# Kernel tuning notes

Measured on AMD Instinct MI355X. Metric: run time of the kernel, lower is better.

The kernel has to match this reference:

```python
import jax, jax.numpy as jnp
import numpy as np

B, N, DIN, DOUT = 8, 2048, 256, 256
ALPHA = 0.2  # leaky relu slope
EPS = 1e-6


def setup_inputs() -> dict:
    key = jax.random.key(0)
    k1, k2, k3, k4 = jax.random.split(key, 4)
    h = jax.random.normal(k1, (B, N, DIN), dtype=jnp.float32)
    adj = jax.random.uniform(k2, (B, N, N), dtype=jnp.float32)
    # xavier_uniform with gain=1.414
    gain = 1.414
    limW = gain * np.sqrt(6.0 / (DIN + DOUT))
    W = jax.random.uniform(k3, (DIN, DOUT), minval=-limW, maxval=limW, dtype=jnp.float32)
    lima = gain * np.sqrt(6.0 / (2 * DOUT + 1))
    a = jax.random.uniform(k4, (2 * DOUT, 1), minval=-lima, maxval=lima, dtype=jnp.float32)
    return {"h": h, "adj": adj, "W": W, "a": a}


def reference(h, adj, W, a):
    # Wh: [B, N, DOUT]
    Wh = jnp.einsum("bnd,df->bnf", h, W)
    # Split additive attention: cat([Wh_i, Wh_j]) @ a == Wh_i @ a1 + Wh_j @ a2
    a1 = a[:DOUT, 0]   # [DOUT]
    a2 = a[DOUT:, 0]   # [DOUT]
    s1 = Wh @ a1       # [B, N] score contribution of source node i
    s2 = Wh @ a2       # [B, N] score contribution of target node j
    e = s1[:, :, None] + s2[:, None, :]           # [B, N, N]
    e = jnp.where(e > 0, e, ALPHA * e)            # leaky relu
    e = e + jnp.log(adj + EPS)                    # soft adjacency mask
    alpha_w = jax.nn.softmax(e, axis=-1)          # [B, N, N]
    # dropout is identity in eval / deterministic reference
    h_prime = jnp.einsum("bij,bjf->bif", alpha_w, Wh)
    return h_prime
```

## Files before the change

### kernel.cpp

```cpp
#include <hip/hip_runtime.h>
#include <hip/hip_bf16.h>
#include <stdint.h>

#define ALPHA_ 0.2f
#define EPS_   1e-6f

typedef __attribute__((ext_vector_type(8))) short  short8;
typedef __attribute__((ext_vector_type(4))) float  float4v;

static __device__ __forceinline__ unsigned short f2bf(float x) {
    union { float f; unsigned int u; } c; c.f = x;
    return (unsigned short)((c.u + 0x7fffu + ((c.u >> 16) & 1u)) >> 16);
}

#define LGKM_BARRIER() asm volatile("s_waitcnt lgkmcnt(0)\n\ts_barrier" ::: "memory")

__global__ __launch_bounds__(256) void k_wt(const float* __restrict__ W,
                                            unsigned short* __restrict__ WT) {
    const int t  = threadIdx.x;
    const int f  = blockIdx.x * 8 + (t >> 5);
    const int d0 = (t & 31) * 8;
    unsigned short v[8];
#pragma unroll
    for (int k = 0; k < 8; ++k) v[k] = f2bf(W[(d0 + k) * 256 + f]);
    uint4 o;
    o.x = (unsigned)v[0] | ((unsigned)v[1] << 16);
    o.y = (unsigned)v[2] | ((unsigned)v[3] << 16);
    o.z = (unsigned)v[4] | ((unsigned)v[5] << 16);
    o.w = (unsigned)v[6] | ((unsigned)v[7] << 16);
    *(uint4*)(WT + f * 256 + d0) = o;
}

__global__ __launch_bounds__(256) void k_wh(const float* __restrict__ h,
                                            const unsigned short* __restrict__ WT,
                                            const float* __restrict__ a,
                                            unsigned short* __restrict__ WhT,
                                            float* __restrict__ s1g,
                                            float* __restrict__ s2g) {
    __shared__ __align__(16) unsigned short A_lds[32][264];
    __shared__ float s1p[32], s2p[32];
    const int t    = threadIdx.x;
    const int lane = t & 63;
    const int wv   = t >> 6;
    const int m    = lane & 15;
    const int quad = lane >> 4;
    const int r0   = blockIdx.x * 32;
    const int b    = r0 >> 11;
    const int j0   = r0 & 2047;

    if (t < 32) { s1p[t] = 0.f; s2p[t] = 0.f; }

#pragma unroll
    for (int k = 0; k < 8; ++k) {
        const int flat = t + k * 256;
        const int r  = flat >> 6;
        const int d4 = flat & 63;
        float4v hv = *(const float4v*)(h + (size_t)(r0 + r) * 256 + d4 * 4);
        uint2 pk;
        pk.x = (unsigned)f2bf(hv.x) | ((unsigned)f2bf(hv.y) << 16);
        pk.y = (unsigned)f2bf(hv.z) | ((unsigned)f2bf(hv.w) << 16);
        *(uint2*)&A_lds[r][d4 * 4] = pk;
    }
    __syncthreads();

    const int fbase = wv * 64;
    float4v acc[2][4];
#pragma unroll
    for (int it = 0; it < 2; ++it)
#pragma unroll
        for (int ft = 0; ft < 4; ++ft)
#pragma unroll
            for (int r = 0; r < 4; ++r) acc[it][ft][r] = 0.f;

    const unsigned short* wtp = WT + (size_t)(fbase + m) * 256 + quad * 8;
    short8 bcur[4], bnxt[4];
#pragma unroll
    for (int ft = 0; ft < 4; ++ft) bcur[ft] = *(const short8*)(wtp + ft * 16 * 256);

#pragma unroll
    for (int kc = 0; kc < 8; ++kc) {
        const int kn = (kc + 1) & 7;
#pragma unroll
        for (int ft = 0; ft < 4; ++ft)
            bnxt[ft] = *(const short8*)(wtp + ft * 16 * 256 + kn * 32);
        short8 af0 = *(const short8*)&A_lds[m][kc * 32 + quad * 8];
        short8 af1 = *(const short8*)&A_lds[16 + m][kc * 32 + quad * 8];
#pragma unroll
        for (int ft = 0; ft < 4; ++ft) {
            acc[0][ft] = __builtin_amdgcn_mfma_f32_16x16x32_bf16(af0, bcur[ft], acc[0][ft], 0, 0, 0);
            acc[1][ft] = __builtin_amdgcn_mfma_f32_16x16x32_bf16(af1, bcur[ft], acc[1][ft], 0, 0, 0);
        }
#pragma unroll
        for (int ft = 0; ft < 4; ++ft) bcur[ft] = bnxt[ft];
    }

    float a1v[4], a2v[4];
#pragma unroll
    for (int ft = 0; ft < 4; ++ft) {
        a1v[ft] = a[fbase + ft * 16 + m];
        a2v[ft] = a[256 + fbase + ft * 16 + m];
    }
#pragma unroll
    for (int it = 0; it < 2; ++it) {
#pragma unroll
        for (int reg = 0; reg < 4; ++reg) {
            float v1 = 0.f, v2 = 0.f;
#pragma unroll
            for (int ft = 0; ft < 4; ++ft) {
                const float c = acc[it][ft][reg];
                v1 = fmaf(c, a1v[ft], v1);
                v2 = fmaf(c, a2v[ft], v2);
            }
            v1 += __shfl_xor(v1, 1); v2 += __shfl_xor(v2, 1);
            v1 += __shfl_xor(v1, 2); v2 += __shfl_xor(v2, 2);
            v1 += __shfl_xor(v1, 4); v2 += __shfl_xor(v2, 4);
            v1 += __shfl_xor(v1, 8); v2 += __shfl_xor(v2, 8);
            if (m == 0) {
                const int row = it * 16 + quad * 4 + reg;
                atomicAdd(&s1p[row], v1);
                atomicAdd(&s2p[row], v2);
            }
        }
    }

    unsigned short* wto = WhT + (size_t)(b * 256 + fbase) * 2048 + j0;
#pragma unroll
    for (int it = 0; it < 2; ++it)
#pragma unroll
        for (int ft = 0; ft < 4; ++ft)
#pragma unroll
            for (int reg = 0; reg < 4; ++reg)
                wto[(size_t)(ft * 16 + m) * 2048 + it * 16 + quad * 4 + reg] =
                    f2bf(acc[it][ft][reg]);

    __syncthreads();
    if (t < 32) {
        s1g[(size_t)b * 2048 + j0 + t] = s1p[t];
        s2g[(size_t)b * 2048 + j0 + t] = s2p[t];
    }
}

__global__ __launch_bounds__(256, 2) void k_attn(const float* __restrict__ adj,
                                                 const unsigned short* __restrict__ WhT,
                                                 const float* __restrict__ s1g,
                                                 const float* __restrict__ s2g,
                                                 float* __restrict__ out) {
    __shared__ __align__(16) unsigned short pbuf[2][32][136];
    __shared__ __align__(16) float s2_lds[2048];
    __shared__ float rsum_lds[32];

    const int t    = threadIdx.x;
    const int lane = t & 63;
    const int wv   = t >> 6;
    const int m    = lane & 15;
    const int quad = lane >> 4;
    const int blk  = blockIdx.x;
    const int b    = blk >> 6;
    const int i0   = (blk & 63) * 32;

    const int ip = t >> 3;
    const int jq = t & 7;

    {
        const float4v* sg = (const float4v*)(s2g + (size_t)b * 2048);
        float4v v0 = sg[t], v1 = sg[t + 256];
        ((float4v*)s2_lds)[t]       = v0;
        ((float4v*)s2_lds)[t + 256] = v1;
    }
    const float s1v = s1g[(size_t)b * 2048 + i0 + ip];
    const float* adjp = adj + (size_t)(b * 2048 + i0 + ip) * 2048 + jq * 4;

    float4v adjv[2][4];
#pragma unroll
    for (int c = 0; c < 4; ++c) adjv[0][c] = *(const float4v*)(adjp + c * 32);

    const size_t bbase = (size_t)(b * 256 + wv * 64 + m) * 2048 + quad * 8;

    float4v acc[2][4];
#pragma unroll
    for (int it = 0; it < 2; ++it)
#pragma unroll
        for (int ft = 0; ft < 4; ++ft)
#pragma unroll
            for (int r = 0; r < 4; ++r) acc[it][ft][r] = 0.f;

    float rsum = 0.f;
    __syncthreads();

#pragma unroll
    for (int step = 0; step < 16; ++step) {
        const int cur   = step & 1, nx = cur ^ 1;
        const int nstep = (step + 1) & 15;

#pragma unroll
        for (int c = 0; c < 4; ++c) {
            const float4v av  = adjv[cur][c];
            const float4v s2v = *(const float4v*)&s2_lds[step * 128 + jq * 4 + c * 32];
            float e0 = s1v + s2v.x, e1 = s1v + s2v.y, e2 = s1v + s2v.z, e3 = s1v + s2v.w;
            e0 = fmaxf(e0, ALPHA_ * e0); e1 = fmaxf(e1, ALPHA_ * e1);
            e2 = fmaxf(e2, ALPHA_ * e2); e3 = fmaxf(e3, ALPHA_ * e3);
            const float p0 = (av.x + EPS_) * __expf(e0);
            const float p1 = (av.y + EPS_) * __expf(e1);
            const float p2 = (av.z + EPS_) * __expf(e2);
            const float p3 = (av.w + EPS_) * __expf(e3);
            rsum += (p0 + p1) + (p2 + p3);
            uint2 pk;
            pk.x = (unsigned)f2bf(p0) | ((unsigned)f2bf(p1) << 16);
            pk.y = (unsigned)f2bf(p2) | ((unsigned)f2bf(p3) << 16);
            *(uint2*)&pbuf[cur][ip][jq * 4 + c * 32] = pk;
        }

#pragma unroll
        for (int c = 0; c < 4; ++c)
            adjv[nx][c] = *(const float4v*)(adjp + (size_t)nstep * 128 + c * 32);

        LGKM_BARRIER();

#pragma unroll
        for (int kc = 0; kc < 4; ++kc) {
            short8 bf[4];
#pragma unroll
            for (int ft = 0; ft < 4; ++ft)
                bf[ft] = *(const short8*)(WhT + bbase + (size_t)ft * 16 * 2048
                                          + step * 128 + kc * 32);
            short8 af0 = *(const short8*)&pbuf[cur][m][kc * 32 + quad * 8];
            short8 af1 = *(const short8*)&pbuf[cur][16 + m][kc * 32 + quad * 8];
#pragma unroll
            for (int ft = 0; ft < 4; ++ft) {
                acc[0][ft] = __builtin_amdgcn_mfma_f32_16x16x32_bf16(af0, bf[ft], acc[0][ft], 0, 0, 0);
                acc[1][ft] = __builtin_amdgcn_mfma_f32_16x16x32_bf16(af1, bf[ft], acc[1][ft], 0, 0, 0);
            }
        }
    }

    float r = rsum;
    r += __shfl_xor(r, 1); r += __shfl_xor(r, 2); r += __shfl_xor(r, 4);
    if (jq == 0) rsum_lds[ip] = r;
    __syncthreads();

#pragma unroll
    for (int it = 0; it < 2; ++it) {
#pragma unroll
        for (int reg = 0; reg < 4; ++reg) {
            const int row = it * 16 + quad * 4 + reg;
            const float inv = 1.0f / rsum_lds[row];
#pragma unroll
            for (int ft = 0; ft < 4; ++ft) {
                out[(size_t)(b * 2048 + i0 + row) * 256 + wv * 64 + ft * 16 + m] =
                    acc[it][ft][reg] * inv;
            }
        }
    }
}

extern "C" void kernel_launch(void* const* d_in, const int* in_sizes, int n_in,
                              void* d_out, int out_size, void* d_ws, size_t ws_size,
                              hipStream_t stream) {
    const float* h   = (const float*)d_in[0];
    const float* adj = (const float*)d_in[1];
    const float* W   = (const float*)d_in[2];
    const float* a   = (const float*)d_in[3];
    float* out = (float*)d_out;

    unsigned short* WhT = (unsigned short*)d_ws;
    unsigned short* WT  = (unsigned short*)((char*)d_ws + 8388608);
    float*          s1  = (float*)((char*)d_ws + 8388608 + 131072);
    float*          s2  = s1 + 16384;

    k_wt  <<<dim3(32),  dim3(256), 0, stream>>>(W, WT);
    k_wh  <<<dim3(512), dim3(256), 0, stream>>>(h, WT, a, WhT, s1, s2);
    k_attn<<<dim3(512), dim3(256), 0, stream>>>(adj, WhT, s1, s2, out);
}
```

Measured before the change: 260.6 us.

## Compute attention probabilities directly in MFMA A-fragment registers, drop LDS and barriers

The attention kernel is rebuilt so each wave computes the softmax numerators for its own 32-row tile straight in the MFMA A-operand register layout. This removes the shared-memory probability buffer and the per-step barriers. Adjacency, s2 and WhT fragments are software-pipelined through double-buffered registers, and each wave now covers 128 output features, so the grid is halved and the launch bound drops to one block per CU. Separately, the Wh kernel stages its transposed bf16 output through LDS so it can write coalesced 16-byte stores. The main risk is higher register pressure and lower occupancy: this memory-bound stream relies on fewer waves to hide latency, and the WhT loads are duplicated across the waves that share a batch.

```diff
diff --git a/kernel.cpp b/kernel.cpp
--- a/kernel.cpp
+++ b/kernel.cpp
@@ -8,12 +8,12 @@
 typedef __attribute__((ext_vector_type(8))) short  short8;
 typedef __attribute__((ext_vector_type(4))) float  float4v;
 
+union U8 { short8 s8; unsigned int u[4]; };
+
 static __device__ __forceinline__ unsigned short f2bf(float x) {
     union { float f; unsigned int u; } c; c.f = x;
     return (unsigned short)((c.u + 0x7fffu + ((c.u >> 16) & 1u)) >> 16);
 }
-
-#define LGKM_BARRIER() asm volatile("s_waitcnt lgkmcnt(0)\n\ts_barrier" ::: "memory")
 
 __global__ __launch_bounds__(256) void k_wt(const float* __restrict__ W,
                                             unsigned short* __restrict__ WT) {
@@ -38,6 +38,7 @@
                                             float* __restrict__ s1g,
                                             float* __restrict__ s2g) {
     __shared__ __align__(16) unsigned short A_lds[32][264];
+    __shared__ __align__(16) unsigned short T_lds[256][40];
     __shared__ float s1p[32], s2p[32];
     const int t    = threadIdx.x;
     const int lane = t & 63;
@@ -123,15 +124,26 @@
         }
     }
 
-    unsigned short* wto = WhT + (size_t)(b * 256 + fbase) * 2048 + j0;
 #pragma unroll
     for (int it = 0; it < 2; ++it)
 #pragma unroll
         for (int ft = 0; ft < 4; ++ft)
 #pragma unroll
             for (int reg = 0; reg < 4; ++reg)
-                wto[(size_t)(ft * 16 + m) * 2048 + it * 16 + quad * 4 + reg] =
+                T_lds[fbase + ft * 16 + m][it * 16 + quad * 4 + reg] =
                     f2bf(acc[it][ft][reg]);
+
+    {
+        uint4 o0 = *(const uint4*)&T_lds[t][0];
+        uint4 o1 = *(const uint4*)&T_lds[t][8];
+        uint4 o2 = *(const uint4*)&T_lds[t][16];
+        uint4 o3 = *(const uint4*)&T_lds[t][24];
+        unsigned short* wto = WhT + ((size_t)(b * 256 + t) * 2048) + j0;
+        *(uint4*)(wto + 0)  = o0;
+        *(uint4*)(wto + 8)  = o1;
+        *(uint4*)(wto + 16) = o2;
+        *(uint4*)(wto + 24) = o3;
+    }
 
     __syncthreads();
     if (t < 32) {
@@ -140,115 +152,114 @@
     }
 }
 
-__global__ __launch_bounds__(256, 2) void k_attn(const float* __restrict__ adj,
+static __device__ __forceinline__ uint2 pquad(float4v av, float4v s2v,
+                                              float s1, float& rs) {
+    float e0 = s1 + s2v.x, e1 = s1 + s2v.y, e2 = s1 + s2v.z, e3 = s1 + s2v.w;
+    e0 = fmaxf(e0, ALPHA_ * e0); e1 = fmaxf(e1, ALPHA_ * e1);
+    e2 = fmaxf(e2, ALPHA_ * e2); e3 = fmaxf(e3, ALPHA_ * e3);
+    const float p0 = (av.x + EPS_) * __expf(e0);
+    const float p1 = (av.y + EPS_) * __expf(e1);
+    const float p2 = (av.z + EPS_) * __expf(e2);
+    const float p3 = (av.w + EPS_) * __expf(e3);
+    rs += (p0 + p1) + (p2 + p3);
+    uint2 r;
+    r.x = (unsigned)f2bf(p0) | ((unsigned)f2bf(p1) << 16);
+    r.y = (unsigned)f2bf(p2) | ((unsigned)f2bf(p3) << 16);
+    return r;
+}
+
+__global__ __launch_bounds__(256, 1) void k_attn(const float* __restrict__ adj,
                                                  const unsigned short* __restrict__ WhT,
                                                  const float* __restrict__ s1g,
                                                  const float* __restrict__ s2g,
                                                  float* __restrict__ out) {
-    __shared__ __align__(16) unsigned short pbuf[2][32][136];
-    __shared__ __align__(16) float s2_lds[2048];
-    __shared__ float rsum_lds[32];
-
-    const int t    = threadIdx.x;
-    const int lane = t & 63;
-    const int wv   = t >> 6;
-    const int m    = lane & 15;
-    const int quad = lane >> 4;
-    const int blk  = blockIdx.x;
-    const int b    = blk >> 6;
-    const int i0   = (blk & 63) * 32;
-
-    const int ip = t >> 3;
-    const int jq = t & 7;
-
-    {
-        const float4v* sg = (const float4v*)(s2g + (size_t)b * 2048);
-        float4v v0 = sg[t], v1 = sg[t + 256];
-        ((float4v*)s2_lds)[t]       = v0;
-        ((float4v*)s2_lds)[t + 256] = v1;
-    }
-    const float s1v = s1g[(size_t)b * 2048 + i0 + ip];
-    const float* adjp = adj + (size_t)(b * 2048 + i0 + ip) * 2048 + jq * 4;
-
-    float4v adjv[2][4];
-#pragma unroll
-    for (int c = 0; c < 4; ++c) adjv[0][c] = *(const float4v*)(adjp + c * 32);
-
-    const size_t bbase = (size_t)(b * 256 + wv * 64 + m) * 2048 + quad * 8;
-
-    float4v acc[2][4];
+    const int t     = threadIdx.x;
+    const int lane  = t & 63;
+    const int wv    = t >> 6;
+    const int m     = lane & 15;
+    const int quad  = lane >> 4;
+    const int fhalf = wv & 1;
+    const int itile = blockIdx.x * 2 + (wv >> 1);
+    const int b     = itile >> 6;
+    const int i0    = (itile & 63) * 32;
+
+    const float* adjp0 = adj + (size_t)(b * 2048 + i0 + m) * 2048 + quad * 8;
+    const float* adjp1 = adjp0 + 16 * 2048;
+    const float* s2p   = s2g + (size_t)b * 2048 + quad * 8;
+    const float  s1v0  = s1g[(size_t)b * 2048 + i0 + m];
+    const float  s1v1  = s1g[(size_t)b * 2048 + i0 + 16 + m];
+
+    const unsigned short* wtp =
+        WhT + (size_t)(b * 256 + fhalf * 128 + m) * 2048 + quad * 8;
+
+    float4v acc[2][8];
 #pragma unroll
     for (int it = 0; it < 2; ++it)
 #pragma unroll
-        for (int ft = 0; ft < 4; ++ft)
+        for (int ft = 0; ft < 8; ++ft)
 #pragma unroll
             for (int r = 0; r < 4; ++r) acc[it][ft][r] = 0.f;
 
-    float rsum = 0.f;
-    __syncthreads();
-
-#pragma unroll
-    for (int step = 0; step < 16; ++step) {
-        const int cur   = step & 1, nx = cur ^ 1;
-        const int nstep = (step + 1) & 15;
-
-#pragma unroll
-        for (int c = 0; c < 4; ++c) {
-            const float4v av  = adjv[cur][c];
-            const float4v s2v = *(const float4v*)&s2_lds[step * 128 + jq * 4 + c * 32];
-            float e0 = s1v + s2v.x, e1 = s1v + s2v.y, e2 = s1v + s2v.z, e3 = s1v + s2v.w;
-            e0 = fmaxf(e0, ALPHA_ * e0); e1 = fmaxf(e1, ALPHA_ * e1);
-            e2 = fmaxf(e2, ALPHA_ * e2); e3 = fmaxf(e3, ALPHA_ * e3);
-            const float p0 = (av.x + EPS_) * __expf(e0);
-            const float p1 = (av.y + EPS_) * __expf(e1);
-            const float p2 = (av.z + EPS_) * __expf(e2);
-            const float p3 = (av.w + EPS_) * __expf(e3);
-            rsum += (p0 + p1) + (p2 + p3);
-            uint2 pk;
-            pk.x = (unsigned)f2bf(p0) | ((unsigned)f2bf(p1) << 16);
-            pk.y = (unsigned)f2bf(p2) | ((unsigned)f2bf(p3) << 16);
-            *(uint2*)&pbuf[cur][ip][jq * 4 + c * 32] = pk;
-        }
-
-#pragma unroll
-        for (int c = 0; c < 4; ++c)
-            adjv[nx][c] = *(const float4v*)(adjp + (size_t)nstep * 128 + c * 32);
-
-        LGKM_BARRIER();
-
-#pragma unroll
-        for (int kc = 0; kc < 4; ++kc) {
-            short8 bf[4];
-#pragma unroll
-            for (int ft = 0; ft < 4; ++ft)
-                bf[ft] = *(const short8*)(WhT + bbase + (size_t)ft * 16 * 2048
-                                          + step * 128 + kc * 32);
-            short8 af0 = *(const short8*)&pbuf[cur][m][kc * 32 + quad * 8];
-            short8 af1 = *(const short8*)&pbuf[cur][16 + m][kc * 32 + quad * 8];
-#pragma unroll
-            for (int ft = 0; ft < 4; ++ft) {
-                acc[0][ft] = __builtin_amdgcn_mfma_f32_16x16x32_bf16(af0, bf[ft], acc[0][ft], 0, 0, 0);
-                acc[1][ft] = __builtin_amdgcn_mfma_f32_16x16x32_bf16(af1, bf[ft], acc[1][ft], 0, 0, 0);
-            }
-        }
-    }
-
-    float r = rsum;
-    r += __shfl_xor(r, 1); r += __shfl_xor(r, 2); r += __shfl_xor(r, 4);
-    if (jq == 0) rsum_lds[ip] = r;
-    __syncthreads();
-
-#pragma unroll
-    for (int it = 0; it < 2; ++it) {
-#pragma unroll
-        for (int reg = 0; reg < 4; ++reg) {
-            const int row = it * 16 + quad * 4 + reg;
-            const float inv = 1.0f / rsum_lds[row];
-#pragma unroll
-            for (int ft = 0; ft < 4; ++ft) {
-                out[(size_t)(b * 2048 + i0 + row) * 256 + wv * 64 + ft * 16 + m] =
-                    acc[it][ft][reg] * inv;
-            }
+    float4v a0buf[2][2], a1buf[2][2], s2buf[2][2];
+    short8  bb[2][8];
+    float   rs0 = 0.f, rs1 = 0.f;
+
+    a0buf[0][0] = *(const float4v*)(adjp0);      a0buf[0][1] = *(const float4v*)(adjp0 + 4);
+    a1buf[0][0] = *(const float4v*)(adjp1);      a1buf[0][1] = *(const float4v*)(adjp1 + 4);
+    a0buf[1][0] = *(const float4v*)(adjp0 + 32); a0buf[1][1] = *(const float4v*)(adjp0 + 36);
+    a1buf[1][0] = *(const float4v*)(adjp1 + 32); a1buf[1][1] = *(const float4v*)(adjp1 + 36);
+    s2buf[0][0] = *(const float4v*)(s2p);        s2buf[0][1] = *(const float4v*)(s2p + 4);
+    s2buf[1][0] = *(const float4v*)(s2p + 32);   s2buf[1][1] = *(const float4v*)(s2p + 36);
+#pragma unroll
+    for (int ft = 0; ft < 8; ++ft)
+        bb[0][ft] = *(const short8*)(wtp + (size_t)ft * 16 * 2048);
+
+#define STEP_BODY(BUF, S)                                                        \
+  {                                                                              \
+    U8 af0u, af1u;                                                               \
+    uint2 q00 = pquad(a0buf[BUF][0], s2buf[BUF][0], s1v0, rs0);                  \
+    uint2 q01 = pquad(a0buf[BUF][1], s2buf[BUF][1], s1v0, rs0);                  \
+    uint2 q10 = pquad(a1buf[BUF][0], s2buf[BUF][0], s1v1, rs1);                  \
+    uint2 q11 = pquad(a1buf[BUF][1], s2buf[BUF][1], s1v1, rs1);                  \
+    af0u.u[0] = q00.x; af0u.u[1] = q00.y; af0u.u[2] = q01.x; af0u.u[3] = q01.y;  \
+    af1u.u[0] = q10.x; af1u.u[1] = q10.y; af1u.u[2] = q11.x; af1u.u[3] = q11.y;  \
+    const int sp = ((S) + 2) & 63;                                               \
+    a0buf[BUF][0] = *(const float4v*)(adjp0 + (size_t)sp * 32);                  \
+    a0buf[BUF][1] = *(const float4v*)(adjp0 + (size_t)sp * 32 + 4);              \
+    a1buf[BUF][0] = *(const float4v*)(adjp1 + (size_t)sp * 32);                  \
+    a1buf[BUF][1] = *(const float4v*)(adjp1 + (size_t)sp * 32 + 4);              \
+    s2buf[BUF][0] = *(const float4v*)(s2p + sp * 32);                            \
+    s2buf[BUF][1] = *(const float4v*)(s2p + sp * 32 + 4);                        \
+    const int sb = ((S) + 1) & 63;                                               \
+    _Pragma("unroll")                                                            \
+    for (int ft = 0; ft < 8; ++ft)                                               \
+      bb[(BUF) ^ 1][ft] = *(const short8*)(wtp + (size_t)ft * 16 * 2048 + sb * 32); \
+    _Pragma("unroll")                                                            \
+    for (int ft = 0; ft < 8; ++ft) {                                             \
+      acc[0][ft] = __builtin_amdgcn_mfma_f32_16x16x32_bf16(af0u.s8, bb[BUF][ft], acc[0][ft], 0, 0, 0); \
+      acc[1][ft] = __builtin_amdgcn_mfma_f32_16x16x32_bf16(af1u.s8, bb[BUF][ft], acc[1][ft], 0, 0, 0); \
+    }                                                                            \
+  }
+
+    for (int s = 0; s < 64; s += 2) {
+        STEP_BODY(0, s)
+        STEP_BODY(1, s + 1)
+    }
+#undef STEP_BODY
+
+    rs0 += __shfl_xor(rs0, 16); rs0 += __shfl_xor(rs0, 32);
+    rs1 += __shfl_xor(rs1, 16); rs1 += __shfl_xor(rs1, 32);
+
+#pragma unroll
+    for (int reg = 0; reg < 4; ++reg) {
+        const int row  = quad * 4 + reg;
+        const float inv0 = 1.0f / __shfl(rs0, row);
+        const float inv1 = 1.0f / __shfl(rs1, row);
+#pragma unroll
+        for (int ft = 0; ft < 8; ++ft) {
+            const int f = fhalf * 128 + ft * 16 + m;
+            out[(size_t)(b * 2048 + i0 + row) * 256 + f]      = acc[0][ft][reg] * inv0;
+            out[(size_t)(b * 2048 + i0 + 16 + row) * 256 + f] = acc[1][ft][reg] * inv1;
         }
     }
 }
@@ -269,5 +280,5 @@
 
     k_wt  <<<dim3(32),  dim3(256), 0, stream>>>(W, WT);
     k_wh  <<<dim3(512), dim3(256), 0, stream>>>(h, WT, a, WhT, s1, s2);
-    k_attn<<<dim3(512), dim3(256), 0, stream>>>(adj, WhT, s1, s2, out);
-}
+    k_attn<<<dim3(256), dim3(256), 0, stream>>>(adj, WhT, s1, s2, out);
+}
```

Result: slower. 287.3 us (+10.2%).

## Stage WhT tiles in LDS via direct global-to-LDS loads and retile attention loop

Applied to the files above, without the earlier changes.

The attention kernel now loads WhT chunks into LDS with global_load_lds, so MFMA B operands come from shared memory instead of per-wave global reads. It uses 64-wide j chunks with single-buffered A/B tiles, reads s2 from global instead of LDS, raises the occupancy hint to 4, and interleaves blocks across batches. The Wh kernel pre-swizzles W into MFMA fragment order and writes WhT through an LDS transpose for coalesced 16-byte stores. The intent is less redundant global traffic and better coalescing. The cost is two barriers per chunk and less software prefetch overlap.

```diff
diff --git a/kernel.cpp b/kernel.cpp
--- a/kernel.cpp
+++ b/kernel.cpp
@@ -8,36 +8,43 @@
 typedef __attribute__((ext_vector_type(8))) short  short8;
 typedef __attribute__((ext_vector_type(4))) float  float4v;
 
+union U8 { short8 s8; unsigned int u[4]; uint4 v4; };
+
 static __device__ __forceinline__ unsigned short f2bf(float x) {
     union { float f; unsigned int u; } c; c.f = x;
     return (unsigned short)((c.u + 0x7fffu + ((c.u >> 16) & 1u)) >> 16);
 }
 
-#define LGKM_BARRIER() asm volatile("s_waitcnt lgkmcnt(0)\n\ts_barrier" ::: "memory")
+#define GLOAD_LDS16(g, l)                                                      \
+    __builtin_amdgcn_global_load_lds(                                          \
+        (const __attribute__((address_space(1))) unsigned int*)(g),            \
+        (__attribute__((address_space(3))) unsigned int*)(l), 16, 0, 0)
 
 __global__ __launch_bounds__(256) void k_wt(const float* __restrict__ W,
-                                            unsigned short* __restrict__ WT) {
-    const int t  = threadIdx.x;
-    const int f  = blockIdx.x * 8 + (t >> 5);
-    const int d0 = (t & 31) * 8;
+                                            unsigned short* __restrict__ WTs) {
+    const int g  = blockIdx.x * 256 + threadIdx.x;
+    const int fb = g >> 9, kc = (g >> 6) & 7, l = g & 63;
+    const int m = l & 15, quad = l >> 4;
+    const int f = fb * 16 + m, d0 = kc * 32 + quad * 8;
     unsigned short v[8];
 #pragma unroll
-    for (int k = 0; k < 8; ++k) v[k] = f2bf(W[(d0 + k) * 256 + f]);
+    for (int i = 0; i < 8; ++i) v[i] = f2bf(W[(d0 + i) * 256 + f]);
     uint4 o;
     o.x = (unsigned)v[0] | ((unsigned)v[1] << 16);
     o.y = (unsigned)v[2] | ((unsigned)v[3] << 16);
     o.z = (unsigned)v[4] | ((unsigned)v[5] << 16);
     o.w = (unsigned)v[6] | ((unsigned)v[7] << 16);
-    *(uint4*)(WT + f * 256 + d0) = o;
+    *(uint4*)(WTs + (size_t)g * 8) = o;
 }
 
 __global__ __launch_bounds__(256) void k_wh(const float* __restrict__ h,
-                                            const unsigned short* __restrict__ WT,
+                                            const unsigned short* __restrict__ WTs,
                                             const float* __restrict__ a,
                                             unsigned short* __restrict__ WhT,
                                             float* __restrict__ s1g,
                                             float* __restrict__ s2g) {
     __shared__ __align__(16) unsigned short A_lds[32][264];
+    __shared__ __align__(16) unsigned short T_lds[256][44];
     __shared__ float s1p[32], s2p[32];
     const int t    = threadIdx.x;
     const int lane = t & 63;
@@ -72,26 +79,18 @@
 #pragma unroll
             for (int r = 0; r < 4; ++r) acc[it][ft][r] = 0.f;
 
-    const unsigned short* wtp = WT + (size_t)(fbase + m) * 256 + quad * 8;
-    short8 bcur[4], bnxt[4];
-#pragma unroll
-    for (int ft = 0; ft < 4; ++ft) bcur[ft] = *(const short8*)(wtp + ft * 16 * 256);
+    const unsigned short* wtb = WTs + (size_t)(wv * 4) * 4096 + lane * 8;
 
 #pragma unroll
     for (int kc = 0; kc < 8; ++kc) {
-        const int kn = (kc + 1) & 7;
-#pragma unroll
-        for (int ft = 0; ft < 4; ++ft)
-            bnxt[ft] = *(const short8*)(wtp + ft * 16 * 256 + kn * 32);
         short8 af0 = *(const short8*)&A_lds[m][kc * 32 + quad * 8];
         short8 af1 = *(const short8*)&A_lds[16 + m][kc * 32 + quad * 8];
 #pragma unroll
         for (int ft = 0; ft < 4; ++ft) {
-            acc[0][ft] = __builtin_amdgcn_mfma_f32_16x16x32_bf16(af0, bcur[ft], acc[0][ft], 0, 0, 0);
-            acc[1][ft] = __builtin_amdgcn_mfma_f32_16x16x32_bf16(af1, bcur[ft], acc[1][ft], 0, 0, 0);
-        }
-#pragma unroll
-        for (int ft = 0; ft < 4; ++ft) bcur[ft] = bnxt[ft];
+            short8 bf = *(const short8*)(wtb + (size_t)ft * 4096 + kc * 512);
+            acc[0][ft] = __builtin_amdgcn_mfma_f32_16x16x32_bf16(af0, bf, acc[0][ft], 0, 0, 0);
+            acc[1][ft] = __builtin_amdgcn_mfma_f32_16x16x32_bf16(af1, bf, acc[1][ft], 0, 0, 0);
+        }
     }
 
     float a1v[4], a2v[4];
@@ -123,15 +122,26 @@
         }
     }
 
-    unsigned short* wto = WhT + (size_t)(b * 256 + fbase) * 2048 + j0;
 #pragma unroll
     for (int it = 0; it < 2; ++it)
 #pragma unroll
         for (int ft = 0; ft < 4; ++ft)
 #pragma unroll
             for (int reg = 0; reg < 4; ++reg)
-                wto[(size_t)(ft * 16 + m) * 2048 + it * 16 + quad * 4 + reg] =
+                T_lds[fbase + ft * 16 + m][it * 16 + quad * 4 + reg] =
                     f2bf(acc[it][ft][reg]);
+
+    {
+        uint4 o0 = *(const uint4*)&T_lds[t][0];
+        uint4 o1 = *(const uint4*)&T_lds[t][8];
+        uint4 o2 = *(const uint4*)&T_lds[t][16];
+        uint4 o3 = *(const uint4*)&T_lds[t][24];
+        unsigned short* wto = WhT + ((size_t)(b * 256 + t) * 2048) + j0;
+        *(uint4*)(wto + 0)  = o0;
+        *(uint4*)(wto + 8)  = o1;
+        *(uint4*)(wto + 16) = o2;
+        *(uint4*)(wto + 24) = o3;
+    }
 
     __syncthreads();
     if (t < 32) {
@@ -140,13 +150,29 @@
     }
 }
 
-__global__ __launch_bounds__(256, 2) void k_attn(const float* __restrict__ adj,
+static __device__ __forceinline__ uint2 pquad(float4v av, float4v s2v,
+                                              float s1, float& rs) {
+    float e0 = s1 + s2v.x, e1 = s1 + s2v.y, e2 = s1 + s2v.z, e3 = s1 + s2v.w;
+    e0 = fmaxf(e0, ALPHA_ * e0); e1 = fmaxf(e1, ALPHA_ * e1);
+    e2 = fmaxf(e2, ALPHA_ * e2); e3 = fmaxf(e3, ALPHA_ * e3);
+    const float p0 = (av.x + EPS_) * __expf(e0);
+    const float p1 = (av.y + EPS_) * __expf(e1);
+    const float p2 = (av.z + EPS_) * __expf(e2);
+    const float p3 = (av.w + EPS_) * __expf(e3);
+    rs += (p0 + p1) + (p2 + p3);
+    uint2 r;
+    r.x = (unsigned)f2bf(p0) | ((unsigned)f2bf(p1) << 16);
+    r.y = (unsigned)f2bf(p2) | ((unsigned)f2bf(p3) << 16);
+    return r;
+}
+
+__global__ __launch_bounds__(256, 4) void k_attn(const float* __restrict__ adj,
                                                  const unsigned short* __restrict__ WhT,
                                                  const float* __restrict__ s1g,
                                                  const float* __restrict__ s2g,
                                                  float* __restrict__ out) {
-    __shared__ __align__(16) unsigned short pbuf[2][32][136];
-    __shared__ __align__(16) float s2_lds[2048];
+    __shared__ __align__(16) unsigned short A_lds[8 * 32 * 8];
+    __shared__ __align__(16) unsigned short B_lds[8 * 256 * 8];
     __shared__ float rsum_lds[32];
 
     const int t    = threadIdx.x;
@@ -154,27 +180,17 @@
     const int wv   = t >> 6;
     const int m    = lane & 15;
     const int quad = lane >> 4;
-    const int blk  = blockIdx.x;
-    const int b    = blk >> 6;
-    const int i0   = (blk & 63) * 32;
-
-    const int ip = t >> 3;
-    const int jq = t & 7;
-
-    {
-        const float4v* sg = (const float4v*)(s2g + (size_t)b * 2048);
-        float4v v0 = sg[t], v1 = sg[t + 256];
-        ((float4v*)s2_lds)[t]       = v0;
-        ((float4v*)s2_lds)[t + 256] = v1;
-    }
-    const float s1v = s1g[(size_t)b * 2048 + i0 + ip];
-    const float* adjp = adj + (size_t)(b * 2048 + i0 + ip) * 2048 + jq * 4;
-
-    float4v adjv[2][4];
-#pragma unroll
-    for (int c = 0; c < 4; ++c) adjv[0][c] = *(const float4v*)(adjp + c * 32);
-
-    const size_t bbase = (size_t)(b * 256 + wv * 64 + m) * 2048 + quad * 8;
+    const int b     = blockIdx.x & 7;
+    const int itile = blockIdx.x >> 3;
+    const int i0    = itile * 32;
+    const int iloc  = t >> 3;
+    const int c     = t & 7;
+    const int fbase = wv * 64;
+
+    const float* adjp = adj + (size_t)(b * 2048 + i0 + iloc) * 2048 + c * 8;
+    const float* s2p  = s2g + (size_t)b * 2048 + c * 8;
+    const float  s1v  = s1g[(size_t)b * 2048 + i0 + iloc];
+    const unsigned short* whb = WhT + (size_t)(b * 256) * 2048;
 
     float4v acc[2][4];
 #pragma unroll
@@ -185,57 +201,55 @@
             for (int r = 0; r < 4; ++r) acc[it][ft][r] = 0.f;
 
     float rsum = 0.f;
-    __syncthreads();
-
-#pragma unroll
-    for (int step = 0; step < 16; ++step) {
-        const int cur   = step & 1, nx = cur ^ 1;
-        const int nstep = (step + 1) & 15;
-
-#pragma unroll
-        for (int c = 0; c < 4; ++c) {
-            const float4v av  = adjv[cur][c];
-            const float4v s2v = *(const float4v*)&s2_lds[step * 128 + jq * 4 + c * 32];
-            float e0 = s1v + s2v.x, e1 = s1v + s2v.y, e2 = s1v + s2v.z, e3 = s1v + s2v.w;
-            e0 = fmaxf(e0, ALPHA_ * e0); e1 = fmaxf(e1, ALPHA_ * e1);
-            e2 = fmaxf(e2, ALPHA_ * e2); e3 = fmaxf(e3, ALPHA_ * e3);
-            const float p0 = (av.x + EPS_) * __expf(e0);
-            const float p1 = (av.y + EPS_) * __expf(e1);
-            const float p2 = (av.z + EPS_) * __expf(e2);
-            const float p3 = (av.w + EPS_) * __expf(e3);
-            rsum += (p0 + p1) + (p2 + p3);
-            uint2 pk;
-            pk.x = (unsigned)f2bf(p0) | ((unsigned)f2bf(p1) << 16);
-            pk.y = (unsigned)f2bf(p2) | ((unsigned)f2bf(p3) << 16);
-            *(uint2*)&pbuf[cur][ip][jq * 4 + c * 32] = pk;
-        }
-
-#pragma unroll
-        for (int c = 0; c < 4; ++c)
-            adjv[nx][c] = *(const float4v*)(adjp + (size_t)nstep * 128 + c * 32);
-
-        LGKM_BARRIER();
-
-#pragma unroll
-        for (int kc = 0; kc < 4; ++kc) {
-            short8 bf[4];
-#pragma unroll
-            for (int ft = 0; ft < 4; ++ft)
-                bf[ft] = *(const short8*)(WhT + bbase + (size_t)ft * 16 * 2048
-                                          + step * 128 + kc * 32);
-            short8 af0 = *(const short8*)&pbuf[cur][m][kc * 32 + quad * 8];
-            short8 af1 = *(const short8*)&pbuf[cur][16 + m][kc * 32 + quad * 8];
+
+    float4v adjc0 = *(const float4v*)(adjp);
+    float4v adjc1 = *(const float4v*)(adjp + 4);
+    float4v s2c0  = *(const float4v*)(s2p);
+    float4v s2c1  = *(const float4v*)(s2p + 4);
+
+    for (int ch = 0; ch < 32; ++ch) {
+        const int j0 = ch * 64;
+
+        U8 au;
+        uint2 qa = pquad(adjc0, s2c0, s1v, rsum);
+        uint2 qb = pquad(adjc1, s2c1, s1v, rsum);
+        au.u[0] = qa.x; au.u[1] = qa.y; au.u[2] = qb.x; au.u[3] = qb.y;
+        *(uint4*)&A_lds[(c * 32 + iloc) * 8] = au.v4;
+
+        const int jn = ((ch + 1) & 31) * 64;
+        adjc0 = *(const float4v*)(adjp + jn);
+        adjc1 = *(const float4v*)(adjp + jn + 4);
+        s2c0  = *(const float4v*)(s2p + jn);
+        s2c1  = *(const float4v*)(s2p + jn + 4);
+
+#pragma unroll
+        for (int k = 0; k < 8; ++k) {
+            const int slot = wv * 512 + k * 64 + lane;
+            const int q = slot >> 8, f = slot & 255;
+            GLOAD_LDS16(whb + (size_t)f * 2048 + j0 + q * 8,
+                        &B_lds[(wv * 512 + k * 64) * 8]);
+        }
+        __syncthreads();
+
+#pragma unroll
+        for (int kc = 0; kc < 2; ++kc) {
+            short8 af0 = *(const short8*)&A_lds[((kc * 4 + quad) * 32 + m) * 8];
+            short8 af1 = *(const short8*)&A_lds[((kc * 4 + quad) * 32 + 16 + m) * 8];
 #pragma unroll
             for (int ft = 0; ft < 4; ++ft) {
-                acc[0][ft] = __builtin_amdgcn_mfma_f32_16x16x32_bf16(af0, bf[ft], acc[0][ft], 0, 0, 0);
-                acc[1][ft] = __builtin_amdgcn_mfma_f32_16x16x32_bf16(af1, bf[ft], acc[1][ft], 0, 0, 0);
-            }
-        }
-    }
-
-    float r = rsum;
-    r += __shfl_xor(r, 1); r += __shfl_xor(r, 2); r += __shfl_xor(r, 4);
-    if (jq == 0) rsum_lds[ip] = r;
+                short8 bf = *(const short8*)
+                    &B_lds[((kc * 4 + quad) * 256 + fbase + ft * 16 + m) * 8];
+                acc[0][ft] = __builtin_amdgcn_mfma_f32_16x16x32_bf16(af0, bf, acc[0][ft], 0, 0, 0);
+                acc[1][ft] = __builtin_amdgcn_mfma_f32_16x16x32_bf16(af1, bf, acc[1][ft], 0, 0, 0);
+            }
+        }
+        __syncthreads();
+    }
+
+    rsum += __shfl_xor(rsum, 1);
+    rsum += __shfl_xor(rsum, 2);
+    rsum += __shfl_xor(rsum, 4);
+    if (c == 0) rsum_lds[iloc] = rsum;
     __syncthreads();
 
 #pragma unroll
@@ -246,7 +260,7 @@
             const float inv = 1.0f / rsum_lds[row];
 #pragma unroll
             for (int ft = 0; ft < 4; ++ft) {
-                out[(size_t)(b * 2048 + i0 + row) * 256 + wv * 64 + ft * 16 + m] =
+                out[(size_t)(b * 2048 + i0 + row) * 256 + fbase + ft * 16 + m] =
                     acc[it][ft][reg] * inv;
             }
         }
@@ -263,11 +277,11 @@
     float* out = (float*)d_out;
 
     unsigned short* WhT = (unsigned short*)d_ws;
-    unsigned short* WT  = (unsigned short*)((char*)d_ws + 8388608);
+    unsigned short* WTs = (unsigned short*)((char*)d_ws + 8388608);
     float*          s1  = (float*)((char*)d_ws + 8388608 + 131072);
     float*          s2  = s1 + 16384;
 
-    k_wt  <<<dim3(32),  dim3(256), 0, stream>>>(W, WT);
-    k_wh  <<<dim3(512), dim3(256), 0, stream>>>(h, WT, a, WhT, s1, s2);
+    k_wt  <<<dim3(32),  dim3(256), 0, stream>>>(W, WTs);
+    k_wh  <<<dim3(512), dim3(256), 0, stream>>>(h, WTs, a, WhT, s1, s2);
     k_attn<<<dim3(512), dim3(256), 0, stream>>>(adj, WhT, s1, s2, out);
 }
```

After: 299.2 us. 14.8% more time.
